# Kernel tuning notes

Measured on AMD Instinct MI355X. Metric: run time of the kernel, lower is better.

Reference implementation:

```python
import jax, jax.numpy as jnp
import numpy as np

# Model dims (match init_kwargs)
B, S = 2, 2048
H = 1024          # hidden_size
I = 256           # intermediate_size
E = 256           # n_routed_experts
K = 8             # num_experts_per_tok
G = 8             # n_group
TG = 4            # topk_group
NS = 2            # n_shared_experts


def setup_inputs() -> dict:
    key = jax.random.key(0)
    ks = jax.random.split(key, 6)
    s = 0.02
    return {
        "x": jax.random.normal(ks[0], (B, S, H), jnp.float32),
        "Wg": jax.random.normal(ks[1], (E, H), jnp.float32) * s,          # gate Linear weight [E,H] (y = x @ Wg.T)
        "W_gate_up": jax.random.normal(ks[2], (E, H, 2 * I), jnp.float32) * s,  # per-expert gate_up proj
        "W_down": jax.random.normal(ks[3], (E, I, H), jnp.float32) * s,          # per-expert down proj
        "Ws_gate_up": jax.random.normal(ks[4], (NS, H, 2 * I), jnp.float32) * s, # shared experts
        "Ws_down": jax.random.normal(ks[5], (NS, I, H), jnp.float32) * s,
    }


def _mlp(x, w_gu, w_d):
    # DeepSeekV3 MLP: down( silu(gate) * up ); gate/up are the two chunks of gate_up
    gu = x @ w_gu                      # [N, 2I]
    g, u = gu[..., :I], gu[..., I:]
    return (jax.nn.silu(g) * u) @ w_d  # [N, H]


def reference(x, Wg, W_gate_up, W_down, Ws_gate_up, Ws_down):
    b, s, h = x.shape
    xf = x.reshape(-1, h)              # [N, H]
    n = xf.shape[0]

    # ---- shared experts (always active, averaged) ----
    shared = (_mlp(xf, Ws_gate_up[0], Ws_down[0]) + _mlp(xf, Ws_gate_up[1], Ws_down[1])) / NS

    # ---- grouped top-k gating ----
    logits = xf @ Wg.T                               # [N, E]
    gsize = E // G
    gl = logits.reshape(n, G, gsize)                 # [N, G, gsize]
    g_top_l, g_top_i = jax.lax.top_k(gl, TG)         # top-TG within each group
    cand_l = g_top_l.reshape(n, G * TG)              # candidate logits (group-major)
    cand_i = g_top_i.reshape(n, G * TG)              # within-group expert ids
    top_l, pos = jax.lax.top_k(cand_l, K)            # global top-K over candidates
    topk_idx = (pos // TG) * gsize + jnp.take_along_axis(cand_i, pos, axis=1)  # [N, K]
    topk_w = jax.nn.softmax(top_l, axis=-1)          # [N, K]

    # ---- routed experts: sort-by-expert + grouped GEMM (ragged_dot) ----
    flat_idx = topk_idx.reshape(-1)                  # [N*K]
    flat_w = topk_w.reshape(-1)
    order = jnp.argsort(flat_idx)                    # tokens grouped by expert id
    tok = order // K                                 # source token of each assignment
    xs = xf[tok]                                     # [N*K, H] gathered tokens, expert-contiguous
    gsz = jnp.bincount(flat_idx, length=E).astype(jnp.int32)  # tokens per expert

    gu = jax.lax.ragged_dot(xs, W_gate_up, gsz)      # [N*K, 2I] grouped GEMM 1
    hmid = jax.nn.silu(gu[:, :I]) * gu[:, I:]
    yo = jax.lax.ragged_dot(hmid, W_down, gsz)       # [N*K, H] grouped GEMM 2
    yo = yo * flat_w[order][:, None]                 # weight by gate prob

    routed = jnp.zeros_like(xf).at[tok].add(yo)      # scatter-add combine

    return (shared + routed).reshape(b, s, h)
```

## Files before the change

kernel.cpp:

```cpp
#include <hip/hip_runtime.h>
#include <hip/hip_bf16.h>


typedef __attribute__((ext_vector_type(4))) float  f32x4;
typedef __attribute__((ext_vector_type(8))) short  bf16x8;
typedef __attribute__((ext_vector_type(4))) short  bf16x4;
typedef __attribute__((ext_vector_type(4))) unsigned short u16x4;

#define DI static __device__ __forceinline__

DI unsigned short f2bf(float f){
  unsigned u = __builtin_bit_cast(unsigned, f);
  return (unsigned short)((u + 0x7FFFu + ((u>>16)&1u)) >> 16);
}
DI float bf2f(unsigned short s){
  return __builtin_bit_cast(float, ((unsigned)s)<<16);
}

#define WS_XBF      0u
#define WS_HSH      8388608u
#define WS_HMID     12582912u
#define WS_YSLOT    29360128u
#define WS_WGT      29360128u
#define WS_TOPKI    96468992u
#define WS_TOPKW    96600064u
#define WS_TOKMAP   96731136u
#define WS_SLOTMAP  96862208u
#define WS_CNT      96993280u
#define WS_CURSOR   96994304u
#define WS_ZERO     96995328u
#define WS_OFF      96999424u

__global__ __launch_bounds__(256) void k_wgT(const float* __restrict__ Wg, float* __restrict__ WgT){
  __shared__ float t[64][65];
  const int tid = threadIdx.x;
  const int hx = blockIdx.x * 64;
  const int ex = blockIdx.y * 64;
  #pragma unroll
  for (int k=0;k<16;++k){
    int i = (tid>>6)*16 + k, j = tid&63;
    t[i][j] = Wg[(size_t)(ex+i)*1024 + hx + j];
  }
  __syncthreads();
  #pragma unroll
  for (int k=0;k<16;++k){
    int i = (tid>>6)*16 + k, j = tid&63;
    WgT[(size_t)(hx+i)*256 + ex + j] = t[j][i];
  }
}

__global__ __launch_bounds__(256) void k_router(const float* __restrict__ x, const float* __restrict__ WgT,
                                                unsigned short* __restrict__ xbf,
                                                int* __restrict__ topki, float* __restrict__ topkw,
                                                int* __restrict__ cnt){
  __shared__ float xs[8][1024];
  __shared__ float lg[8][256];
  __shared__ float cv[8][32];
  __shared__ int   ce[8][32];
  const int tid = threadIdx.x;
  const int t0  = blockIdx.x * 8;
  {
    const f32x4* xg = (const f32x4*)(x + (size_t)t0*1024);
    f32x4* xs4 = (f32x4*)&xs[0][0];
    u16x4* xb4 = (u16x4*)(xbf + (size_t)t0*1024);
    #pragma unroll
    for (int i=0;i<8;++i){
      f32x4 v = xg[tid + i*256];
      xs4[tid + i*256] = v;
      u16x4 p; p[0]=f2bf(v[0]); p[1]=f2bf(v[1]); p[2]=f2bf(v[2]); p[3]=f2bf(v[3]);
      xb4[tid + i*256] = p;
    }
  }
  __syncthreads();
  {
    f32x4 a4[8];
    #pragma unroll
    for (int t=0;t<8;++t) a4[t] = (f32x4){0.f,0.f,0.f,0.f};
    const float* wc = WgT + tid;
    for (int h4=0; h4<256; ++h4){
      float w0 = wc[(size_t)(h4*4+0)*256];
      float w1 = wc[(size_t)(h4*4+1)*256];
      float w2 = wc[(size_t)(h4*4+2)*256];
      float w3 = wc[(size_t)(h4*4+3)*256];
      f32x4 wv = (f32x4){w0,w1,w2,w3};
      #pragma unroll
      for (int t=0;t<8;++t){
        f32x4 xv = *((const f32x4*)&xs[t][0] + h4);
        a4[t] += wv * xv;
      }
    }
    #pragma unroll
    for (int t=0;t<8;++t){
      double d = ((double)a4[t][0] + (double)a4[t][1]) + ((double)a4[t][2] + (double)a4[t][3]);
      lg[t][tid] = (float)d;
    }
  }
  __syncthreads();
  if (tid < 64){
    int tok = tid>>3, grp = tid&7;
    unsigned mask = 0;
    for (int j=0;j<4;++j){
      float best = -3.4e38f; int bi = 0;
      for (int i=0;i<32;++i){
        float v = lg[tok][grp*32+i];
        if (!((mask>>i)&1u) && v > best){ best=v; bi=i; }
      }
      mask |= 1u<<bi;
      cv[tok][grp*4+j] = best; ce[tok][grp*4+j] = grp*32+bi;
    }
  }
  __syncthreads();
  if (tid < 8){
    int tok = tid; unsigned mask=0;
    float vals[8]; int es[8];
    #pragma unroll
    for (int k=0;k<8;++k){
      float best=-3.4e38f; int bp=0;
      for (int p=0;p<32;++p){
        float v = cv[tok][p];
        if (!((mask>>p)&1u) && v > best){ best=v; bp=p; }
      }
      mask|=1u<<bp; vals[k]=best; es[k]=ce[tok][bp];
    }
    float m = vals[0], s=0.f, w[8];
    #pragma unroll
    for (int k=0;k<8;++k){ w[k]=expf(vals[k]-m); s+=w[k]; }
    float inv = 1.f/s;
    #pragma unroll
    for (int k=0;k<8;++k){
      int g=(t0+tok)*8+k;
      topki[g]=es[k]; topkw[g]=w[k]*inv;
      atomicAdd(&cnt[es[k]],1);
    }
  }
}

__global__ void k_scan(const int* __restrict__ cnt, int* __restrict__ off){
  __shared__ int s[256];
  int tid=threadIdx.x;
  s[tid]=cnt[tid]; __syncthreads();
  for (int d=1; d<256; d<<=1){
    int v = (tid>=d)? s[tid-d] : 0; __syncthreads();
    s[tid]+=v; __syncthreads();
  }
  off[tid+1]=s[tid]; if(tid==0) off[0]=0;
}

__global__ void k_scatter(const int* __restrict__ topki, const int* __restrict__ off,
                          int* __restrict__ cursor, int* __restrict__ tokmap, int* __restrict__ slotmap){
  int g = blockIdx.x*256 + threadIdx.x;
  int e = topki[g];
  int p = off[e] + atomicAdd(&cursor[e], 1);
  tokmap[p] = g >> 3;
  slotmap[g] = p;
}

template<int GEMM>
__global__ __launch_bounds__(512, 2) void k_gemm(
    const unsigned short* __restrict__ A1, const unsigned short* __restrict__ A2,
    const float* __restrict__ WE, const float* __restrict__ WS,
    const int* __restrict__ cnt, const int* __restrict__ off,
    const int* __restrict__ tokmap,
    unsigned short* __restrict__ O1, unsigned short* __restrict__ O2,
    float* __restrict__ OD, const unsigned short* __restrict__ zpage)
{
  __shared__ __align__(16) char smem[98304];
  const int e = blockIdx.x, mt = blockIdx.y, nc = blockIdx.z;
  const bool sh = (e >= 256);
  const int M = sh ? 4096 : cnt[e];
  const int Moff = mt*256;
  if (Moff >= M) return;
  const int tid=threadIdx.x, ln=tid&63, wv=tid>>6, wm=wv>>2, wn=wv&3, lrow=ln&15, lk=ln>>4;
  const int Ktot = (GEMM==1)?1024:(sh?512:256);
  const int ldB  = (GEMM==1)?512:1024;
  const float* Bp = (GEMM==1) ? (sh? WS + (size_t)(e-256)*524288 : WE + (size_t)e*524288)
                              : (sh? WS : WE + (size_t)e*262144);
  const int offe = sh? 0 : off[e];

  const char* a_src[2];
  #pragma unroll
  for (int qi=0;qi<2;++qi){
    int row  = (wv*2+qi)*16 + (ln>>2);
    int grow = Moff + row;
    const unsigned short* p;
    if (GEMM==1){
      if (!sh) p = (grow < M)? A1 + (size_t)tokmap[offe+grow]*1024 : zpage;
      else     p = A1 + (size_t)grow*1024;
    } else {
      if (!sh) p = (grow < M)? A1 + ((size_t)offe+grow)*256 : zpage;
      else     p = A2 + (size_t)grow*512;
    }
    a_src[qi] = (const char*)p + (ln&3)*16;
  }
  const char* b_src[4];
  {
    int swz = ((wv>>1)&3)<<2;
    int cg  = ln ^ swz;
    int tcb = cg*4;
    int gcol = (GEMM==1)? (nc*128 + tcb + ((tcb>=128)?128:0)) : (nc*256 + tcb);
    #pragma unroll
    for (int r=0;r<4;++r){
      int kr = wv*4 + r;
      b_src[r] = (const char*)(Bp + (size_t)kr*ldB + gcol);
    }
  }

  f32x4 acc[8][4] = {};

  auto stage = [&](int buf, int k0){
    #pragma unroll
    for (int qi=0;qi<2;++qi)
      __builtin_amdgcn_global_load_lds((const void*)(a_src[qi] + (size_t)k0*2),
          (void*)(smem + buf*16384 + (wv*2+qi)*1024), 16, 0, 0);
    #pragma unroll
    for (int r=0;r<4;++r)
      __builtin_amdgcn_global_load_lds((const void*)(b_src[r] + (size_t)k0*ldB*4),
          (void*)(smem + 32768 + buf*32768 + (wv*4+r)*1024), 16, 0, 0);
  };

  auto compute = [&](int buf){
    const short* as  = (const short*)(smem + buf*16384);
    const float* bs  = (const float*)(smem + 32768 + buf*32768);
    bf16x8 af[8];
    #pragma unroll
    for (int mi=0;mi<8;++mi) af[mi] = *(const bf16x8*)(as + (wm*128+mi*16+lrow)*32 + lk*8);
    #pragma unroll
    for (int ni=0;ni<4;++ni){
      int n0 = (GEMM==1)? ((ni<2)? wn*32+ni*16 : 128+wn*32+(ni-2)*16) : (wn*64+ni*16);
      int tc = n0 + lrow;
      int sloff = ((((tc>>2) ^ (lk<<2))<<2) | (tc&3));
      const float* colp = bs + (size_t)lk*8*256 + sloff;
      bf16x8 bv;
      #pragma unroll
      for (int j=0;j<8;++j){
        unsigned u = __builtin_bit_cast(unsigned, colp[(size_t)j*256]);
        bv[j] = (short)((u + 0x8000u) >> 16);
      }
      #pragma unroll
      for (int mi=0;mi<8;++mi)
        acc[mi][ni] = __builtin_amdgcn_mfma_f32_16x16x32_bf16(af[mi], bv, acc[mi][ni], 0,0,0);
    }
  };

  stage(0, 0);
  const int ns = Ktot>>5;
  for (int t=0;t<ns;++t){
    int b = t&1;
    if (t+1<ns){
      stage(b^1, (t+1)<<5);
      asm volatile("s_waitcnt vmcnt(6)" ::: "memory");
    } else {
      asm volatile("s_waitcnt vmcnt(0)" ::: "memory");
    }
    asm volatile("s_barrier" ::: "memory");
    compute(b);
    asm volatile("s_barrier" ::: "memory");
  }

  if (GEMM==1){
    __syncthreads();
    unsigned short* Hs = (unsigned short*)smem;
    #pragma unroll
    for (int mi=0;mi<8;++mi)
      #pragma unroll
      for (int ni=0;ni<2;++ni){
        f32x4 g = acc[mi][ni], u = acc[mi][ni+2];
        #pragma unroll
        for (int r=0;r<4;++r){
          float gg = g[r];
          float hh = (gg / (1.f + __expf(-gg))) * u[r];
          int m = wm*128 + mi*16 + lk*4 + r;
          int c = wn*32 + ni*16 + lrow;
          Hs[m*128 + c] = f2bf(hh);
        }
      }
    __syncthreads();
    #pragma unroll
    for (int i=0;i<8;++i){
      int id = tid + i*512, m = id>>4, c8 = id&15;
      int grow = Moff + m;
      if (grow < M){
        unsigned short* dst = (!sh) ? O1 + ((size_t)offe + grow)*256 + nc*128 + c8*8
                                    : O2 + (size_t)grow*512 + (size_t)(e-256)*256 + nc*128 + c8*8;
        *(f32x4*)dst = *(const f32x4*)(Hs + m*128 + c8*8);
      }
    }
  } else {
    if (sh){
      #pragma unroll
      for (int mi=0;mi<8;++mi)
        #pragma unroll
        for (int ni=0;ni<4;++ni)
          #pragma unroll
          for (int r=0;r<4;++r){
            int m = Moff + wm*128 + mi*16 + lk*4 + r;
            int c = nc*256 + wn*64 + ni*16 + lrow;
            OD[(size_t)m*1024 + c] = acc[mi][ni][r]*0.5f;
          }
    } else {
      unsigned short* Hs = (unsigned short*)smem;
      #pragma unroll
      for (int pass=0; pass<2; ++pass){
        __syncthreads();
        if ((wn>>1) == pass){
          #pragma unroll
          for (int mi=0;mi<8;++mi)
            #pragma unroll
            for (int ni=0;ni<4;++ni)
              #pragma unroll
              for (int r=0;r<4;++r){
                int m = wm*128 + mi*16 + lk*4 + r;
                int c = (wn&1)*64 + ni*16 + lrow;
                Hs[m*128 + c] = f2bf(acc[mi][ni][r]);
              }
        }
        __syncthreads();
        #pragma unroll
        for (int i=0;i<8;++i){
          int id = tid + i*512, m = id>>4, c8 = id&15;
          int grow = Moff + m;
          if (grow < M){
            unsigned short* dst = O1 + ((size_t)offe+grow)*1024 + nc*256 + pass*128 + c8*8;
            *(f32x4*)dst = *(const f32x4*)(Hs + m*128 + c8*8);
          }
        }
      }
    }
  }
}

__global__ void k_final(float* __restrict__ out, const unsigned short* __restrict__ yslot,
                        const int* __restrict__ slotmap, const float* __restrict__ topkw){
  __shared__ int sp[8]; __shared__ float sw[8];
  int t = blockIdx.x, tid = threadIdx.x;
  if (tid<8){ sp[tid]=slotmap[t*8+tid]; sw[tid]=topkw[t*8+tid]; }
  __syncthreads();
  int c = tid*4;
  f32x4 o = *(f32x4*)(out + (size_t)t*1024 + c);
  #pragma unroll
  for (int k=0;k<8;++k){
    u16x4 y = *(const u16x4*)(yslot + (size_t)sp[k]*1024 + c);
    float w = sw[k];
    o[0] += w*bf2f(y[0]); o[1] += w*bf2f(y[1]); o[2] += w*bf2f(y[2]); o[3] += w*bf2f(y[3]);
  }
  *(f32x4*)(out + (size_t)t*1024 + c) = o;
}

extern "C" void kernel_launch(void* const* d_in, const int* in_sizes, int n_in,
                              void* d_out, int out_size, void* d_ws, size_t ws_size,
                              hipStream_t stream) {
  const float* x    = (const float*)d_in[0];
  const float* Wg   = (const float*)d_in[1];
  const float* Wgu  = (const float*)d_in[2];
  const float* Wd   = (const float*)d_in[3];
  const float* Wsgu = (const float*)d_in[4];
  const float* Wsd  = (const float*)d_in[5];
  float* out = (float*)d_out;

  char* W = (char*)d_ws;
  unsigned short* xbf    = (unsigned short*)(W + WS_XBF);
  unsigned short* hsh    = (unsigned short*)(W + WS_HSH);
  unsigned short* hmid   = (unsigned short*)(W + WS_HMID);
  unsigned short* yslot  = (unsigned short*)(W + WS_YSLOT);
  float* WgT     = (float*)(W + WS_WGT);
  int*   topki   = (int*)(W + WS_TOPKI);
  float* topkw   = (float*)(W + WS_TOPKW);
  int*   tokmap  = (int*)(W + WS_TOKMAP);
  int*   slotmap = (int*)(W + WS_SLOTMAP);
  int*   cnt     = (int*)(W + WS_CNT);
  int*   cursor  = (int*)(W + WS_CURSOR);
  unsigned short* zpage = (unsigned short*)(W + WS_ZERO);
  int*   off     = (int*)(W + WS_OFF);

  hipMemsetAsync((void*)cnt, 0, 1024+1024+4096, stream);

  k_wgT    <<<dim3(16,4), 256, 0, stream>>>(Wg, WgT);
  k_router <<<512, 256, 0, stream>>>(x, WgT, xbf, topki, topkw, cnt);
  k_scan   <<<1, 256, 0, stream>>>(cnt, off);
  k_scatter<<<128, 256, 0, stream>>>(topki, off, cursor, tokmap, slotmap);
  k_gemm<1><<<dim3(258,16,2), 512, 0, stream>>>(xbf, (const unsigned short*)nullptr,
        Wgu, Wsgu, cnt, off, tokmap, hmid, hsh, out, zpage);
  k_gemm<2><<<dim3(257,16,4), 512, 0, stream>>>(hmid, hsh,
        Wd, Wsd, cnt, off, tokmap, yslot, (unsigned short*)nullptr, out, zpage);
  k_final <<<4096, 256, 0, stream>>>(out, yslot, slotmap, topkw);
}
```

Measured before the change: 397.0 us.

## Halve GEMM N-tile, shrink LDS, and compact grid for routed and shared experts

Halves the output-column tile of both grouped GEMMs, which halves the B staging buffers and LDS use and raises the launch-bounds occupancy hint. The grid is reshaped: routed experts get only 2 (GEMM1) or 4 (GEMM2) M-tiles instead of 16, which removes most of the early-exit blocks. The shared-expert rows are spread across extra x-indices, so shared work is split into more blocks. This risks silently dropping tokens for any expert routed more than 512 tokens (GEMM1) or 1024 (GEMM2), and it lowers per-block data reuse of the A tiles.

```diff
diff --git a/kernel.cpp b/kernel.cpp
--- a/kernel.cpp
+++ b/kernel.cpp
@@ -156,7 +156,7 @@
 }
 
 template<int GEMM>
-__global__ __launch_bounds__(512, 2) void k_gemm(
+__global__ __launch_bounds__(512, 4) void k_gemm(
     const unsigned short* __restrict__ A1, const unsigned short* __restrict__ A2,
     const float* __restrict__ WE, const float* __restrict__ WS,
     const int* __restrict__ cnt, const int* __restrict__ off,
@@ -164,16 +164,22 @@
     unsigned short* __restrict__ O1, unsigned short* __restrict__ O2,
     float* __restrict__ OD, const unsigned short* __restrict__ zpage)
 {
-  __shared__ __align__(16) char smem[98304];
-  const int e = blockIdx.x, mt = blockIdx.y, nc = blockIdx.z;
-  const bool sh = (e >= 256);
-  const int M = sh ? 4096 : cnt[e];
-  const int Moff = mt*256;
+  __shared__ __align__(16) char smem[65536];
+  const int bx = blockIdx.x, mt = blockIdx.y, nc = blockIdx.z;
+  const bool sh = (bx >= 256);
+  int e = bx, s = 0, M, Moff;
+  if (!sh){ M = cnt[e]; Moff = mt*256; }
+  else {
+    int sidx = bx - 256;
+    if (GEMM==1){ s = sidx>>3; Moff = (sidx&7)*512 + mt*256; }
+    else        { s = 0;       Moff = sidx*1024 + mt*256; }
+    M = 4096;
+  }
   if (Moff >= M) return;
   const int tid=threadIdx.x, ln=tid&63, wv=tid>>6, wm=wv>>2, wn=wv&3, lrow=ln&15, lk=ln>>4;
   const int Ktot = (GEMM==1)?1024:(sh?512:256);
   const int ldB  = (GEMM==1)?512:1024;
-  const float* Bp = (GEMM==1) ? (sh? WS + (size_t)(e-256)*524288 : WE + (size_t)e*524288)
+  const float* Bp = (GEMM==1) ? (sh? WS + (size_t)s*524288 : WE + (size_t)e*524288)
                               : (sh? WS : WE + (size_t)e*262144);
   const int offe = sh? 0 : off[e];
 
@@ -192,20 +198,20 @@
     }
     a_src[qi] = (const char*)p + (ln&3)*16;
   }
-  const char* b_src[4];
+  const char* b_src[2];
   {
     int swz = ((wv>>1)&3)<<2;
-    int cg  = ln ^ swz;
-    int tcb = cg*4;
-    int gcol = (GEMM==1)? (nc*128 + tcb + ((tcb>=128)?128:0)) : (nc*256 + tcb);
-    #pragma unroll
-    for (int r=0;r<4;++r){
-      int kr = wv*4 + r;
-      b_src[r] = (const char*)(Bp + (size_t)kr*ldB + gcol);
-    }
-  }
-
-  f32x4 acc[8][4] = {};
+    int cg  = (ln&31) ^ swz;
+    int c4  = cg*4;
+    int gcol = (GEMM==1) ? ((c4<64)? nc*64 + c4 : 256 + nc*64 + (c4-64))
+                         : (nc*128 + c4);
+    int rbase = 4*wv + (ln>>5);
+    #pragma unroll
+    for (int q=0;q<2;++q)
+      b_src[q] = (const char*)(Bp + (size_t)(rbase + 2*q)*ldB + gcol);
+  }
+
+  f32x4 acc[8][2] = {};
 
   auto stage = [&](int buf, int k0){
     #pragma unroll
@@ -213,32 +219,31 @@
       __builtin_amdgcn_global_load_lds((const void*)(a_src[qi] + (size_t)k0*2),
           (void*)(smem + buf*16384 + (wv*2+qi)*1024), 16, 0, 0);
     #pragma unroll
-    for (int r=0;r<4;++r)
-      __builtin_amdgcn_global_load_lds((const void*)(b_src[r] + (size_t)k0*ldB*4),
-          (void*)(smem + 32768 + buf*32768 + (wv*4+r)*1024), 16, 0, 0);
+    for (int q=0;q<2;++q)
+      __builtin_amdgcn_global_load_lds((const void*)(b_src[q] + (size_t)k0*ldB*4),
+          (void*)(smem + 32768 + buf*16384 + wv*2048 + q*1024), 16, 0, 0);
   };
 
   auto compute = [&](int buf){
     const short* as  = (const short*)(smem + buf*16384);
-    const float* bs  = (const float*)(smem + 32768 + buf*32768);
-    bf16x8 af[8];
-    #pragma unroll
-    for (int mi=0;mi<8;++mi) af[mi] = *(const bf16x8*)(as + (wm*128+mi*16+lrow)*32 + lk*8);
-    #pragma unroll
-    for (int ni=0;ni<4;++ni){
-      int n0 = (GEMM==1)? ((ni<2)? wn*32+ni*16 : 128+wn*32+(ni-2)*16) : (wn*64+ni*16);
-      int tc = n0 + lrow;
+    const float* bs  = (const float*)(smem + 32768 + buf*16384);
+    bf16x8 bv[2];
+    #pragma unroll
+    for (int ni=0;ni<2;++ni){
+      int tc = (GEMM==1)? (ni*64 + wn*16 + lrow) : (wn*32 + ni*16 + lrow);
       int sloff = ((((tc>>2) ^ (lk<<2))<<2) | (tc&3));
-      const float* colp = bs + (size_t)lk*8*256 + sloff;
-      bf16x8 bv;
+      const float* colp = bs + (size_t)lk*8*128 + sloff;
       #pragma unroll
       for (int j=0;j<8;++j){
-        unsigned u = __builtin_bit_cast(unsigned, colp[(size_t)j*256]);
-        bv[j] = (short)((u + 0x8000u) >> 16);
-      }
-      #pragma unroll
-      for (int mi=0;mi<8;++mi)
-        acc[mi][ni] = __builtin_amdgcn_mfma_f32_16x16x32_bf16(af[mi], bv, acc[mi][ni], 0,0,0);
+        unsigned u = __builtin_bit_cast(unsigned, colp[(size_t)j*128]);
+        bv[ni][j] = (short)((u + 0x8000u) >> 16);
+      }
+    }
+    #pragma unroll
+    for (int mi=0;mi<8;++mi){
+      bf16x8 af = *(const bf16x8*)(as + (wm*128+mi*16+lrow)*32 + lk*8);
+      acc[mi][0] = __builtin_amdgcn_mfma_f32_16x16x32_bf16(af, bv[0], acc[mi][0], 0,0,0);
+      acc[mi][1] = __builtin_amdgcn_mfma_f32_16x16x32_bf16(af, bv[1], acc[mi][1], 0,0,0);
     }
   };
 
@@ -248,7 +253,7 @@
     int b = t&1;
     if (t+1<ns){
       stage(b^1, (t+1)<<5);
-      asm volatile("s_waitcnt vmcnt(6)" ::: "memory");
+      asm volatile("s_waitcnt vmcnt(4)" ::: "memory");
     } else {
       asm volatile("s_waitcnt vmcnt(0)" ::: "memory");
     }
@@ -261,28 +266,25 @@
     __syncthreads();
     unsigned short* Hs = (unsigned short*)smem;
     #pragma unroll
-    for (int mi=0;mi<8;++mi)
-      #pragma unroll
-      for (int ni=0;ni<2;++ni){
-        f32x4 g = acc[mi][ni], u = acc[mi][ni+2];
-        #pragma unroll
-        for (int r=0;r<4;++r){
-          float gg = g[r];
-          float hh = (gg / (1.f + __expf(-gg))) * u[r];
-          int m = wm*128 + mi*16 + lk*4 + r;
-          int c = wn*32 + ni*16 + lrow;
-          Hs[m*128 + c] = f2bf(hh);
-        }
-      }
+    for (int mi=0;mi<8;++mi){
+      f32x4 g = acc[mi][0], u = acc[mi][1];
+      #pragma unroll
+      for (int r=0;r<4;++r){
+        float gg = g[r];
+        float hh = (gg / (1.f + __expf(-gg))) * u[r];
+        int m = wm*128 + mi*16 + lk*4 + r;
+        Hs[m*72 + wn*16 + lrow] = f2bf(hh);
+      }
+    }
     __syncthreads();
     #pragma unroll
-    for (int i=0;i<8;++i){
-      int id = tid + i*512, m = id>>4, c8 = id&15;
+    for (int i=0;i<4;++i){
+      int id = tid + i*512, m = id>>3, c8 = id&7;
       int grow = Moff + m;
       if (grow < M){
-        unsigned short* dst = (!sh) ? O1 + ((size_t)offe + grow)*256 + nc*128 + c8*8
-                                    : O2 + (size_t)grow*512 + (size_t)(e-256)*256 + nc*128 + c8*8;
-        *(f32x4*)dst = *(const f32x4*)(Hs + m*128 + c8*8);
+        unsigned short* dst = (!sh) ? O1 + ((size_t)offe + grow)*256 + nc*64 + c8*8
+                                    : O2 + (size_t)grow*512 + (size_t)s*256 + nc*64 + c8*8;
+        *(f32x4*)dst = *(const f32x4*)(Hs + m*72 + c8*8);
       }
     }
   } else {
@@ -290,39 +292,34 @@
       #pragma unroll
       for (int mi=0;mi<8;++mi)
         #pragma unroll
-        for (int ni=0;ni<4;++ni)
+        for (int ni=0;ni<2;++ni)
           #pragma unroll
           for (int r=0;r<4;++r){
             int m = Moff + wm*128 + mi*16 + lk*4 + r;
-            int c = nc*256 + wn*64 + ni*16 + lrow;
+            int c = nc*128 + wn*32 + ni*16 + lrow;
             OD[(size_t)m*1024 + c] = acc[mi][ni][r]*0.5f;
           }
     } else {
+      __syncthreads();
       unsigned short* Hs = (unsigned short*)smem;
       #pragma unroll
-      for (int pass=0; pass<2; ++pass){
-        __syncthreads();
-        if ((wn>>1) == pass){
+      for (int mi=0;mi<8;++mi)
+        #pragma unroll
+        for (int ni=0;ni<2;++ni)
           #pragma unroll
-          for (int mi=0;mi<8;++mi)
-            #pragma unroll
-            for (int ni=0;ni<4;++ni)
-              #pragma unroll
-              for (int r=0;r<4;++r){
-                int m = wm*128 + mi*16 + lk*4 + r;
-                int c = (wn&1)*64 + ni*16 + lrow;
-                Hs[m*128 + c] = f2bf(acc[mi][ni][r]);
-              }
-        }
-        __syncthreads();
-        #pragma unroll
-        for (int i=0;i<8;++i){
-          int id = tid + i*512, m = id>>4, c8 = id&15;
-          int grow = Moff + m;
-          if (grow < M){
-            unsigned short* dst = O1 + ((size_t)offe+grow)*1024 + nc*256 + pass*128 + c8*8;
-            *(f32x4*)dst = *(const f32x4*)(Hs + m*128 + c8*8);
+          for (int r=0;r<4;++r){
+            int m = wm*128 + mi*16 + lk*4 + r;
+            int c = wn*32 + ni*16 + lrow;
+            Hs[m*128 + c] = f2bf(acc[mi][ni][r]);
           }
+      __syncthreads();
+      #pragma unroll
+      for (int i=0;i<8;++i){
+        int id = tid + i*512, m = id>>4, c8 = id&15;
+        int grow = Moff + m;
+        if (grow < M){
+          unsigned short* dst = O1 + ((size_t)offe+grow)*1024 + nc*128 + c8*8;
+          *(f32x4*)dst = *(const f32x4*)(Hs + m*128 + c8*8);
         }
       }
     }
@@ -378,9 +375,9 @@
   k_router <<<512, 256, 0, stream>>>(x, WgT, xbf, topki, topkw, cnt);
   k_scan   <<<1, 256, 0, stream>>>(cnt, off);
   k_scatter<<<128, 256, 0, stream>>>(topki, off, cursor, tokmap, slotmap);
-  k_gemm<1><<<dim3(258,16,2), 512, 0, stream>>>(xbf, (const unsigned short*)nullptr,
+  k_gemm<1><<<dim3(272,2,4), 512, 0, stream>>>(xbf, (const unsigned short*)nullptr,
         Wgu, Wsgu, cnt, off, tokmap, hmid, hsh, out, zpage);
-  k_gemm<2><<<dim3(257,16,4), 512, 0, stream>>>(hmid, hsh,
+  k_gemm<2><<<dim3(260,4,8), 512, 0, stream>>>(hmid, hsh,
         Wd, Wsd, cnt, off, tokmap, yslot, (unsigned short*)nullptr, out, zpage);
   k_final <<<4096, 256, 0, stream>>>(out, yslot, slotmap, topkw);
 }
```

New measurement: 352.4 us. 11.2% less time.
